# Kernel tuning notes

Measured on AMD Instinct MI355X. Metric: run time of the kernel, lower is better.

The kernel has to match this reference:

```python
import jax, jax.numpy as jnp
import numpy as np

B, D, K, A, P = 4096, 512, 128, 32, 16  # batch, theta dim, mixture comps, alpha dim, hutchinson probes


def setup_inputs() -> dict:
    key = jax.random.key(0)
    k1, k2, k3, k4 = jax.random.split(key, 4)
    thetas = jax.random.normal(k1, (B, D), dtype=jnp.float32)
    alpha = jax.random.normal(k2, (K, A), dtype=jnp.float32)
    W = jax.random.normal(k3, (A, D), dtype=jnp.float32) / jnp.sqrt(jnp.float32(A))
    v_int = jax.random.randint(k4, (P, B, D), 0, 2, dtype=jnp.int32)  # -> Rademacher via 2v-1
    return {"thetas": thetas, "alpha": alpha, "W": W, "v_int": v_int,
            "N_dataset": 100000, "K_alpha_samples": K}


def _log_density(thetas, alpha, W, N_dataset, K_alpha):
    # Tempered Gaussian mixture: mu_k = alpha_k @ W;
    # logp_b = (N/(N+1)) * (logsumexp_k -0.5||theta_b - mu_k||^2 - log K)
    mu = alpha @ W                                        # [K, D]
    # ||t - mu||^2 expanded to avoid a [B,K,D] intermediate
    sq = (jnp.sum(thetas * thetas, -1, keepdims=True)
          - 2.0 * thetas @ mu.T
          + jnp.sum(mu * mu, -1)[None, :])                # [B, K]
    temper = jnp.float32(N_dataset) / (jnp.float32(N_dataset) + 1.0)
    return temper * (jax.nn.logsumexp(-0.5 * sq, axis=1) - jnp.log(jnp.float32(K_alpha)))


def reference(thetas, alpha, W, v_int, N_dataset, K_alpha_samples):
    v = (2 * v_int - 1).astype(thetas.dtype)              # [P, B, D] Rademacher

    def logp_sum(t):
        return jnp.sum(_log_density(t, alpha, W, N_dataset, K_alpha_samples))

    score = jax.grad(logp_sum)                            # gradiente wrt thetas
    g = score(thetas)                                     # [B, D]

    # Hutchinson trace of the per-sample Hessian via forward-over-reverse HVPs,
    # batched over probes (fuses the torch per-probe autograd.grad loop).
    def hvp(vi):
        return jax.jvp(score, (thetas,), (vi,))[1]        # [B, D]

    Hv = jax.vmap(hvp)(v)                                 # [P, B, D]
    traces = jnp.mean(jnp.sum(v * Hv, axis=-1), axis=0)   # [B]

    loss = 0.5 * jnp.sum(g * g, axis=-1) + traces         # [B]
    return jnp.mean(loss)
```

## Files before the change

### kernel.cpp

```cpp
#include <hip/hip_runtime.h>
#include <hip/hip_bf16.h>
#include <stdint.h>

#define Bsz 4096
#define Dn  512
#define Kn  128
#define Pn  16
#define An  32
#define TB  16

typedef __attribute__((ext_vector_type(4))) float  floatx4;
typedef __attribute__((ext_vector_type(8))) short  shortx8;

__device__ __forceinline__ unsigned short f2bf(float x) {
    union { float f; uint32_t u; } v; v.f = x;
    uint32_t u = v.u;
    uint32_t r = (u + 0x7FFFu + ((u >> 16) & 1u)) >> 16;
    return (unsigned short)r;
}

__global__ __launch_bounds__(256) void k_mu(const float* __restrict__ alpha,
                                            const float* __restrict__ W,
                                            unsigned short* __restrict__ mu_bf,
                                            unsigned short* __restrict__ mu_t,
                                            float* __restrict__ munorm,
                                            float* __restrict__ out) {
    __shared__ float al[An];
    __shared__ float red[4];
    int k = blockIdx.x, t = threadIdx.x;
    if (k == 0 && t == 0) *out = 0.f;
    if (t < An) al[t] = alpha[k * An + t];
    __syncthreads();
    int d0 = t, d1 = t + 256;
    float a0 = 0.f, a1 = 0.f;
#pragma unroll
    for (int a = 0; a < An; ++a) {
        float av = al[a];
        a0 = fmaf(av, W[a * Dn + d0], a0);
        a1 = fmaf(av, W[a * Dn + d1], a1);
    }
    unsigned short h0 = f2bf(a0), h1 = f2bf(a1);
    mu_bf[k * Dn + d0] = h0;  mu_bf[k * Dn + d1] = h1;
    mu_t[d0 * Kn + k] = h0;   mu_t[d1 * Kn + k] = h1;
    float nrm = a0 * a0 + a1 * a1;
#pragma unroll
    for (int msk = 1; msk < 64; msk <<= 1) nrm += __shfl_xor(nrm, msk);
    if ((t & 63) == 0) red[t >> 6] = nrm;
    __syncthreads();
    if (t == 0) munorm[k] = red[0] + red[1] + red[2] + red[3];
}

__global__ __launch_bounds__(512, 4) void k_main(
    const float* __restrict__ thetas,
    const int* __restrict__ v_int,
    const unsigned short* __restrict__ mu_bf,
    const float* __restrict__ munorm,
    const unsigned short* __restrict__ mu_t,
    const int* __restrict__ Np,
    float* __restrict__ out)
{
    __shared__ short vt[2][TB][520];
    __shared__ float S_l[TB][132];
    __shared__ float w_l[TB][132];
    __shared__ short wbf[TB][136];
    __shared__ float part[2][8][TB][2];
    __shared__ float thn[TB];
    __shared__ float SwS[TB];

    const int tid = threadIdx.x;
    const int lane = tid & 63;
    const int wv = tid >> 6;
    const int m = lane & 15;
    const int q = lane >> 4;

    const int tileb = blockIdx.x >> 1;
    const int phalf = blockIdx.x & 1;
    const int b0 = tileb * TB;
    const int p0 = phalf * 8;

    const float Nf = (float)(*Np);
    const float temper = Nf / (Nf + 1.0f);

    const int kcol = wv * 16 + m;
    shortx8 mufrag[16];
    {
        const unsigned short* mb = mu_bf + (size_t)kcol * Dn + q * 8;
#pragma unroll
        for (int dc = 0; dc < 16; ++dc)
            mufrag[dc] = *(const shortx8*)(mb + dc * 32);
    }

    const int r = tid >> 5;
    const int c0 = (tid & 31) * 16;
    const size_t PB = (size_t)Bsz * Dn;
    const int* vrow = v_int + (size_t)(b0 + r) * Dn + c0;

    int4 buf[4];
    {
        const int4* g = (const int4*)(vrow + (size_t)p0 * PB);
#pragma unroll
        for (int j = 0; j < 4; ++j) buf[j] = g[j];
    }
    {
        const float4* tg = (const float4*)(thetas + (size_t)(b0 + r) * Dn + c0);
        float tn = 0.f;
#pragma unroll
        for (int j = 0; j < 4; ++j) {
            float4 f = tg[j];
            tn += f.x * f.x + f.y * f.y + f.z * f.z + f.w * f.w;
            short4 h;
            h.x = (short)f2bf(f.x); h.y = (short)f2bf(f.y);
            h.z = (short)f2bf(f.z); h.w = (short)f2bf(f.w);
            *(short4*)&vt[0][r][c0 + j * 4] = h;
        }
#pragma unroll
        for (int msk = 1; msk < 32; msk <<= 1) tn += __shfl_xor(tn, msk);
        if ((tid & 31) == 0) thn[r] = tn;
    }
    __syncthreads();

    {
        floatx4 acc = {0.f, 0.f, 0.f, 0.f};
#pragma unroll
        for (int dc = 0; dc < 16; ++dc) {
            shortx8 a = *(const shortx8*)&vt[0][m][dc * 32 + q * 8];
            acc = __builtin_amdgcn_mfma_f32_16x16x32_bf16(a, mufrag[dc], acc, 0, 0, 0);
        }
#pragma unroll
        for (int i = 0; i < 4; ++i) S_l[q * 4 + i][kcol] = acc[i];
    }
    __syncthreads();

    {
        const int b = tid >> 5, s = tid & 31;
        float l[4];
        float mx = -3.4e38f;
        float tnb = thn[b];
#pragma unroll
        for (int j = 0; j < 4; ++j) {
            int k = s + 32 * j;
            l[j] = -0.5f * (tnb - 2.f * S_l[b][k] + munorm[k]);
            mx = fmaxf(mx, l[j]);
        }
#pragma unroll
        for (int msk = 1; msk < 32; msk <<= 1) mx = fmaxf(mx, __shfl_xor(mx, msk));
        float se = 0.f, ses = 0.f;
        float e[4];
#pragma unroll
        for (int j = 0; j < 4; ++j) {
            int k = s + 32 * j;
            e[j] = __expf(l[j] - mx);
            se += e[j];
            ses += e[j] * S_l[b][k];
        }
#pragma unroll
        for (int msk = 1; msk < 32; msk <<= 1) { se += __shfl_xor(se, msk); ses += __shfl_xor(ses, msk); }
        float inv = 1.f / se;
#pragma unroll
        for (int j = 0; j < 4; ++j) {
            int k = s + 32 * j;
            float wvv = e[j] * inv;
            w_l[b][k] = wvv;
            wbf[b][k] = (short)f2bf(wvv);
        }
        if (s == 0) SwS[b] = ses * inv;
    }
    __syncthreads();

    {
        float sg[4] = {0.f, 0.f, 0.f, 0.f};
#pragma unroll
        for (int ct = 0; ct < 4; ++ct) {
            const unsigned short* mt = mu_t + (size_t)(wv * 64 + ct * 16 + m) * Kn + q * 8;
            floatx4 acc = {0.f, 0.f, 0.f, 0.f};
#pragma unroll
            for (int kc = 0; kc < 4; ++kc) {
                shortx8 a = *(const shortx8*)&wbf[m][kc * 32 + q * 8];
                shortx8 bfr = *(const shortx8*)(mt + kc * 32);
                acc = __builtin_amdgcn_mfma_f32_16x16x32_bf16(a, bfr, acc, 0, 0, 0);
            }
#pragma unroll
            for (int i = 0; i < 4; ++i) sg[i] += acc[i] * acc[i];
        }
#pragma unroll
        for (int msk = 1; msk < 16; msk <<= 1) {
#pragma unroll
            for (int i = 0; i < 4; ++i) sg[i] += __shfl_xor(sg[i], msk);
        }
        if (m == 0) {
#pragma unroll
            for (int i = 0; i < 4; ++i) part[0][wv][q * 4 + i][0] = sg[i];
        }
    }
    __syncthreads();

    float lossA = 0.f, tracc = 0.f;
    if (tid < TB) {
        float wGw = 0.f;
#pragma unroll
        for (int w8 = 0; w8 < 8; ++w8) wGw += part[0][w8][tid][0];
        if (phalf == 0)
            lossA = 0.5f * temper * temper * (wGw - 2.f * SwS[tid] + thn[tid])
                    - temper * (float)Dn;
    }

#pragma unroll
    for (int p = 0; p < 8; ++p) {
#pragma unroll
        for (int j = 0; j < 4; ++j) {
            int4 w4 = buf[j];
            uint32_t lo = 0xBF80BF80u ^ ((uint32_t)w4.x << 15) ^ ((uint32_t)w4.y << 31);
            uint32_t hi = 0xBF80BF80u ^ ((uint32_t)w4.z << 15) ^ ((uint32_t)w4.w << 31);
            uint2 pk; pk.x = lo; pk.y = hi;
            *(uint2*)&vt[p & 1][r][c0 + j * 4] = pk;
        }
        __syncthreads();
        if (p < 7) {
            const int4* g = (const int4*)(vrow + (size_t)(p0 + p + 1) * PB);
#pragma unroll
            for (int j = 0; j < 4; ++j) buf[j] = g[j];
        }
        if (p > 0 && tid < TB) {
            float S1 = 0.f, S2 = 0.f;
#pragma unroll
            for (int w8 = 0; w8 < 8; ++w8) {
                S1 += part[(p - 1) & 1][w8][tid][0];
                S2 += part[(p - 1) & 1][w8][tid][1];
            }
            tracc += S1 - S2 * S2;
        }
        floatx4 acc = {0.f, 0.f, 0.f, 0.f};
#pragma unroll
        for (int dc = 0; dc < 16; ++dc) {
            shortx8 a = *(const shortx8*)&vt[p & 1][m][dc * 32 + q * 8];
            acc = __builtin_amdgcn_mfma_f32_16x16x32_bf16(a, mufrag[dc], acc, 0, 0, 0);
        }
        float s1[4], s2[4];
#pragma unroll
        for (int i = 0; i < 4; ++i) {
            float T = acc[i];
            float wt = w_l[q * 4 + i][kcol];
            s1[i] = wt * T * T;
            s2[i] = wt * T;
        }
#pragma unroll
        for (int msk = 1; msk < 16; msk <<= 1) {
#pragma unroll
            for (int i = 0; i < 4; ++i) {
                s1[i] += __shfl_xor(s1[i], msk);
                s2[i] += __shfl_xor(s2[i], msk);
            }
        }
        if (m == 0) {
#pragma unroll
            for (int i = 0; i < 4; ++i) {
                part[p & 1][wv][q * 4 + i][0] = s1[i];
                part[p & 1][wv][q * 4 + i][1] = s2[i];
            }
        }
    }
    __syncthreads();
    if (tid < TB) {
        float S1 = 0.f, S2 = 0.f;
#pragma unroll
        for (int w8 = 0; w8 < 8; ++w8) {
            S1 += part[1][w8][tid][0];
            S2 += part[1][w8][tid][1];
        }
        tracc += S1 - S2 * S2;
        float res = temper * tracc * (1.0f / (float)Pn) + lossA;
#pragma unroll
        for (int msk = 1; msk < 16; msk <<= 1) res += __shfl_xor(res, msk);
        if (tid == 0) atomicAdd(out, res * (1.0f / (float)Bsz));
    }
}

extern "C" void kernel_launch(void* const* d_in, const int* in_sizes, int n_in,
                              void* d_out, int out_size, void* d_ws, size_t ws_size,
                              hipStream_t stream) {
    const float* thetas = (const float*)d_in[0];
    const float* alpha  = (const float*)d_in[1];
    const float* W      = (const float*)d_in[2];
    const int*   v_int  = (const int*)d_in[3];
    const int*   Np     = (const int*)d_in[4];

    char* ws = (char*)d_ws;
    unsigned short* mu_bf  = (unsigned short*)ws;
    float*          munorm = (float*)(ws + 131072);
    unsigned short* mu_t   = (unsigned short*)(ws + 131072 + 1024);

    float* out = (float*)d_out;
    k_mu  <<<dim3(Kn),  dim3(256), 0, stream>>>(alpha, W, mu_bf, mu_t, munorm, out);
    k_main<<<dim3(512), dim3(512), 0, stream>>>(thetas, v_int, mu_bf, munorm, mu_t, Np, out);
}
```

Baseline: 218.2 us.

## Use DPP row reductions, hoist mixture weights, widen probe LDS stores

```diff
diff --git a/kernel.cpp b/kernel.cpp
--- a/kernel.cpp
+++ b/kernel.cpp
@@ -17,6 +17,14 @@
     uint32_t u = v.u;
     uint32_t r = (u + 0x7FFFu + ((u >> 16) & 1u)) >> 16;
     return (unsigned short)r;
+}
+
+__device__ __forceinline__ float rowsum16(float x) {
+    x += __int_as_float(__builtin_amdgcn_update_dpp(0, __float_as_int(x), 0xB1, 0xF, 0xF, false));
+    x += __int_as_float(__builtin_amdgcn_update_dpp(0, __float_as_int(x), 0x4E, 0xF, 0xF, false));
+    x += __int_as_float(__builtin_amdgcn_update_dpp(0, __float_as_int(x), 0x124, 0xF, 0xF, false));
+    x += __int_as_float(__builtin_amdgcn_update_dpp(0, __float_as_int(x), 0x128, 0xF, 0xF, false));
+    return x;
 }
 
 __global__ __launch_bounds__(256) void k_mu(const float* __restrict__ alpha,
@@ -183,15 +191,16 @@
             for (int i = 0; i < 4; ++i) sg[i] += acc[i] * acc[i];
         }
 #pragma unroll
-        for (int msk = 1; msk < 16; msk <<= 1) {
-#pragma unroll
-            for (int i = 0; i < 4; ++i) sg[i] += __shfl_xor(sg[i], msk);
-        }
+        for (int i = 0; i < 4; ++i) sg[i] = rowsum16(sg[i]);
         if (m == 0) {
 #pragma unroll
             for (int i = 0; i < 4; ++i) part[0][wv][q * 4 + i][0] = sg[i];
         }
     }
+
+    float wt4[4];
+#pragma unroll
+    for (int i = 0; i < 4; ++i) wt4[i] = w_l[q * 4 + i][kcol];
     __syncthreads();
 
     float lossA = 0.f, tracc = 0.f;
@@ -207,12 +216,14 @@
 #pragma unroll
     for (int p = 0; p < 8; ++p) {
 #pragma unroll
-        for (int j = 0; j < 4; ++j) {
-            int4 w4 = buf[j];
-            uint32_t lo = 0xBF80BF80u ^ ((uint32_t)w4.x << 15) ^ ((uint32_t)w4.y << 31);
-            uint32_t hi = 0xBF80BF80u ^ ((uint32_t)w4.z << 15) ^ ((uint32_t)w4.w << 31);
-            uint2 pk; pk.x = lo; pk.y = hi;
-            *(uint2*)&vt[p & 1][r][c0 + j * 4] = pk;
+        for (int j = 0; j < 2; ++j) {
+            int4 a = buf[2 * j], b = buf[2 * j + 1];
+            uint32_t l0 = 0xBF80BF80u ^ ((uint32_t)a.x << 15) ^ ((uint32_t)a.y << 31);
+            uint32_t l1 = 0xBF80BF80u ^ ((uint32_t)a.z << 15) ^ ((uint32_t)a.w << 31);
+            uint32_t l2 = 0xBF80BF80u ^ ((uint32_t)b.x << 15) ^ ((uint32_t)b.y << 31);
+            uint32_t l3 = 0xBF80BF80u ^ ((uint32_t)b.z << 15) ^ ((uint32_t)b.w << 31);
+            uint4 pk; pk.x = l0; pk.y = l1; pk.z = l2; pk.w = l3;
+            *(uint4*)&vt[p & 1][r][c0 + j * 8] = pk;
         }
         __syncthreads();
         if (p < 7) {
@@ -239,17 +250,13 @@
 #pragma unroll
         for (int i = 0; i < 4; ++i) {
             float T = acc[i];
-            float wt = w_l[q * 4 + i][kcol];
-            s1[i] = wt * T * T;
-            s2[i] = wt * T;
-        }
-#pragma unroll
-        for (int msk = 1; msk < 16; msk <<= 1) {
-#pragma unroll
-            for (int i = 0; i < 4; ++i) {
-                s1[i] += __shfl_xor(s1[i], msk);
-                s2[i] += __shfl_xor(s2[i], msk);
-            }
+            s1[i] = wt4[i] * T * T;
+            s2[i] = wt4[i] * T;
+        }
+#pragma unroll
+        for (int i = 0; i < 4; ++i) {
+            s1[i] = rowsum16(s1[i]);
+            s2[i] = rowsum16(s2[i]);
         }
         if (m == 0) {
 #pragma unroll
```

Result: no change. 220.1 us (+0.9%).
